# Optimization experiments

Measured on AMD Instinct MI355X. Metric: run time of the kernel, lower is better.

## Reference

```python
import jax, jax.numpy as jnp
import numpy as np

# Grid spacing (CartesianGrid3D.dx / .dy)
DX = 1000.0
DY = 1000.0
WENO_EPS = 1e-6  # classic Jiang-Shu smoothness regularizer

NZ, NY, NX = 32, 1024, 1024


def _weno5_recon(qm2, qm1, q0, qp1, qp2):
    """Classic WENO5 (Jiang-Shu) reconstruction of q at the i+1/2 face,
    left-biased (stencil centered on cell i)."""
    c1312 = 13.0 / 12.0
    b0 = c1312 * (qm2 - 2.0 * qm1 + q0) ** 2 + 0.25 * (qm2 - 4.0 * qm1 + 3.0 * q0) ** 2
    b1 = c1312 * (qm1 - 2.0 * q0 + qp1) ** 2 + 0.25 * (qm1 - qp1) ** 2
    b2 = c1312 * (q0 - 2.0 * qp1 + qp2) ** 2 + 0.25 * (3.0 * q0 - 4.0 * qp1 + qp2) ** 2
    a0 = 0.1 / (WENO_EPS + b0) ** 2
    a1 = 0.6 / (WENO_EPS + b1) ** 2
    a2 = 0.3 / (WENO_EPS + b2) ** 2
    p0 = (2.0 * qm2 - 7.0 * qm1 + 11.0 * q0) / 6.0
    p1 = (-qm1 + 5.0 * q0 + 2.0 * qp1) / 6.0
    p2 = (2.0 * q0 + 5.0 * qp1 - qp2) / 6.0
    return (a0 * p0 + a1 * p1 + a2 * p2) / (a0 + a1 + a2)


def _weno5_flux(q, vel, axis):
    """Upwinded WENO5 flux vel * q_face at face i+1/2 along `axis`.
    Edge-padded so the flux array has the same shape as q (faithful to
    recon.weno5_x / weno5_y producing full-shape flux arrays whose interior
    is consumed by the divergence)."""
    q = jnp.moveaxis(q, axis, -1)
    vel = jnp.moveaxis(vel, axis, -1)
    n = q.shape[-1]
    pad = [(0, 0)] * (q.ndim - 1) + [(2, 3)]
    qp = jnp.pad(q, pad, mode='edge')
    sl = lambda o: qp[..., o:o + n]
    qm2, qm1, q0, qp1, qp2, qp3 = sl(0), sl(1), sl(2), sl(3), sl(4), sl(5)
    q_left = _weno5_recon(qm2, qm1, q0, qp1, qp2)          # upwind for vel >= 0
    q_right = _weno5_recon(qp3, qp2, qp1, q0, qm1)         # mirrored, vel < 0
    f = vel * jnp.where(vel >= 0.0, q_left, q_right)
    return jnp.moveaxis(f, -1, axis)


def setup_inputs() -> dict:
    key = jax.random.key(0)
    kh, ku, kv = jax.random.split(key, 3)
    h = jax.random.normal(kh, (NZ, NY, NX), dtype=jnp.float32)
    u = jax.random.normal(ku, (NZ, NY, NX), dtype=jnp.float32)
    v = jax.random.normal(kv, (NZ, NY, NX), dtype=jnp.float32)
    return {"h": h, "u": u, "v": v}


def reference(h, u, v):
    # fe: flux through east face (x), fn: flux through north face (y)
    fe = _weno5_flux(h, u, axis=2)
    fn = _weno5_flux(h, v, axis=1)
    div = ((fe[1:-1, 2:-2, 2:-2] - fe[1:-1, 2:-2, 1:-3]) / DX
           + (fn[1:-1, 2:-2, 2:-2] - fn[1:-1, 1:-3, 2:-2]) / DY)
    out = jnp.zeros_like(h)
    out = out.at[1:-1, 2:-2, 2:-2].set(-div)
    return out
```

## Files before the change

### kernel.cpp

```cpp
#include <hip/hip_runtime.h>

#define NZ 32
#define NY 1024
#define NX 1024

__device__ __forceinline__ float rcpf(float x) { return __builtin_amdgcn_rcpf(x); }

__device__ __forceinline__ float weno5(float qm2, float qm1, float q0, float qp1, float qp2) {
    const float c1312 = 13.0f / 12.0f;
    float t0 = qm2 - 2.0f * qm1 + q0;
    float u0 = qm2 - 4.0f * qm1 + 3.0f * q0;
    float b0 = c1312 * t0 * t0 + 0.25f * u0 * u0;
    float t1 = qm1 - 2.0f * q0 + qp1;
    float u1 = qm1 - qp1;
    float b1 = c1312 * t1 * t1 + 0.25f * u1 * u1;
    float t2 = q0 - 2.0f * qp1 + qp2;
    float u2 = 3.0f * q0 - 4.0f * qp1 + qp2;
    float b2 = c1312 * t2 * t2 + 0.25f * u2 * u2;
    float e0 = 1e-6f + b0;
    float e1 = 1e-6f + b1;
    float e2 = 1e-6f + b2;
    float a0 = 0.1f * rcpf(e0 * e0);
    float a1 = 0.6f * rcpf(e1 * e1);
    float a2 = 0.3f * rcpf(e2 * e2);
    const float c16 = 1.0f / 6.0f;
    float p0 = (2.0f * qm2 - 7.0f * qm1 + 11.0f * q0) * c16;
    float p1 = (-qm1 + 5.0f * q0 + 2.0f * qp1) * c16;
    float p2 = (2.0f * q0 + 5.0f * qp1 - qp2) * c16;
    return (a0 * p0 + a1 * p1 + a2 * p2) * rcpf(a0 + a1 + a2);
}

__device__ __forceinline__ float upwind_flux(float vel, float qm2, float qm1, float q0,
                                             float qp1, float qp2, float qp3) {
    bool up = vel >= 0.0f;
    float s0 = up ? qm2 : qp3;
    float s1 = up ? qm1 : qp2;
    float s2 = up ? q0  : qp1;
    float s3 = up ? qp1 : q0;
    float s4 = up ? qp2 : qm1;
    return vel * weno5(s0, s1, s2, s3, s4);
}

__global__ __launch_bounds__(256) void adv_kernel(const float* __restrict__ h,
                                                  const float* __restrict__ u,
                                                  const float* __restrict__ v,
                                                  float* __restrict__ out) {
    int x = blockIdx.x * blockDim.x + threadIdx.x;
    int y = blockIdx.y;
    int z = blockIdx.z;
    size_t base = ((size_t)z * NY + y) * NX;
    size_t idx = base + x;

    bool interior = (z >= 1) && (z <= NZ - 2) && (y >= 2) && (y <= NY - 3) &&
                    (x >= 2) && (x <= NX - 3);
    if (!interior) {
        out[idx] = 0.0f;
        return;
    }

    const float* row = h + base;
    float hx[7];
#pragma unroll
    for (int k = 0; k < 7; ++k) {
        int xx = x - 3 + k;
        xx = xx < 0 ? 0 : (xx > NX - 1 ? NX - 1 : xx);
        hx[k] = row[xx];
    }
    float fe_hi = upwind_flux(u[idx],     hx[1], hx[2], hx[3], hx[4], hx[5], hx[6]);
    float fe_lo = upwind_flux(u[idx - 1], hx[0], hx[1], hx[2], hx[3], hx[4], hx[5]);

    float hy[7];
#pragma unroll
    for (int k = 0; k < 7; ++k) {
        int yy = y - 3 + k;
        yy = yy < 0 ? 0 : (yy > NY - 1 ? NY - 1 : yy);
        hy[k] = h[((size_t)z * NY + yy) * NX + x];
    }
    float fn_hi = upwind_flux(v[idx],      hy[1], hy[2], hy[3], hy[4], hy[5], hy[6]);
    float fn_lo = upwind_flux(v[idx - NX], hy[0], hy[1], hy[2], hy[3], hy[4], hy[5]);

    const float inv_dx = 1.0f / 1000.0f;
    const float inv_dy = 1.0f / 1000.0f;
    out[idx] = -((fe_hi - fe_lo) * inv_dx + (fn_hi - fn_lo) * inv_dy);
}

extern "C" void kernel_launch(void* const* d_in, const int* in_sizes, int n_in,
                              void* d_out, int out_size, void* d_ws, size_t ws_size,
                              hipStream_t stream) {
    const float* h = (const float*)d_in[0];
    const float* u = (const float*)d_in[1];
    const float* v = (const float*)d_in[2];
    float* out = (float*)d_out;

    dim3 block(256, 1, 1);
    dim3 grid(NX / 256, NY, NZ);
    adv_kernel<<<grid, block, 0, stream>>>(h, u, v, out);
}
```

Measured before the change: 444.2 us.

## Tile h in shared memory, reuse face fluxes across rows and cells

Each block now processes 8 rows and stages an h tile with a 3-cell halo in LDS. Each x-face and y-face flux is computed once and shared between neighbouring cells, instead of being computed twice per cell (hi and lo). The WENO weights are also rewritten to use products of the other smoothness terms, which avoids three reciprocals. This removes redundant WENO evaluations and repeated global loads, at the cost of LDS use, two barriers and more registers. Without the regularised reciprocal, products of squared betas can overflow or underflow.

```diff
diff --git a/kernel.cpp b/kernel.cpp
--- a/kernel.cpp
+++ b/kernel.cpp
@@ -3,6 +3,10 @@
 #define NZ 32
 #define NY 1024
 #define NX 1024
+#define KY 8
+#define BX 256
+#define HS 264
+#define FS 258
 
 __device__ __forceinline__ float rcpf(float x) { return __builtin_amdgcn_rcpf(x); }
 
@@ -17,12 +21,11 @@
     float t2 = q0 - 2.0f * qp1 + qp2;
     float u2 = 3.0f * q0 - 4.0f * qp1 + qp2;
     float b2 = c1312 * t2 * t2 + 0.25f * u2 * u2;
-    float e0 = 1e-6f + b0;
-    float e1 = 1e-6f + b1;
-    float e2 = 1e-6f + b2;
-    float a0 = 0.1f * rcpf(e0 * e0);
-    float a1 = 0.6f * rcpf(e1 * e1);
-    float a2 = 0.3f * rcpf(e2 * e2);
+    float e0 = 1e-6f + b0, e1 = 1e-6f + b1, e2 = 1e-6f + b2;
+    float s12 = e1 * e2, s02 = e0 * e2, s01 = e0 * e1;
+    float a0 = 0.1f * (s12 * s12);
+    float a1 = 0.6f * (s02 * s02);
+    float a2 = 0.3f * (s01 * s01);
     const float c16 = 1.0f / 6.0f;
     float p0 = (2.0f * qm2 - 7.0f * qm1 + 11.0f * q0) * c16;
     float p1 = (-qm1 + 5.0f * q0 + 2.0f * qp1) * c16;
@@ -41,47 +44,80 @@
     return vel * weno5(s0, s1, s2, s3, s4);
 }
 
+__device__ __forceinline__ int clampi(int a, int lo, int hi) {
+    return a < lo ? lo : (a > hi ? hi : a);
+}
+
 __global__ __launch_bounds__(256) void adv_kernel(const float* __restrict__ h,
                                                   const float* __restrict__ u,
                                                   const float* __restrict__ v,
                                                   float* __restrict__ out) {
-    int x = blockIdx.x * blockDim.x + threadIdx.x;
-    int y = blockIdx.y;
-    int z = blockIdx.z;
-    size_t base = ((size_t)z * NY + y) * NX;
-    size_t idx = base + x;
+    __shared__ float hs[(KY + 6) * HS];
+    __shared__ float fs[KY * FS];
 
-    bool interior = (z >= 1) && (z <= NZ - 2) && (y >= 2) && (y <= NY - 3) &&
-                    (x >= 2) && (x <= NX - 3);
-    if (!interior) {
-        out[idx] = 0.0f;
+    const int tid = threadIdx.x;
+    const int x0 = blockIdx.x * BX;
+    const int y0 = blockIdx.y * KY;
+    const int z  = blockIdx.z;
+    const int x = x0 + tid;
+    const size_t zbase = (size_t)z * NY * NX;
+
+    if (z == 0 || z == NZ - 1) {
+#pragma unroll
+        for (int r = 0; r < KY; ++r)
+            out[zbase + (size_t)(y0 + r) * NX + x] = 0.0f;
         return;
     }
 
-    const float* row = h + base;
-    float hx[7];
 #pragma unroll
-    for (int k = 0; k < 7; ++k) {
-        int xx = x - 3 + k;
-        xx = xx < 0 ? 0 : (xx > NX - 1 ? NX - 1 : xx);
-        hx[k] = row[xx];
+    for (int r = 0; r < KY + 6; ++r) {
+        int yy = clampi(y0 - 3 + r, 0, NY - 1);
+        const float* hrow = h + zbase + (size_t)yy * NX;
+        for (int c = tid; c < HS; c += BX) {
+            int xx = clampi(x0 - 3 + c, 0, NX - 1);
+            hs[r * HS + c] = hrow[xx];
+        }
     }
-    float fe_hi = upwind_flux(u[idx],     hx[1], hx[2], hx[3], hx[4], hx[5], hx[6]);
-    float fe_lo = upwind_flux(u[idx - 1], hx[0], hx[1], hx[2], hx[3], hx[4], hx[5]);
+    __syncthreads();
 
-    float hy[7];
+    float hc[KY + 6];
 #pragma unroll
-    for (int k = 0; k < 7; ++k) {
-        int yy = y - 3 + k;
-        yy = yy < 0 ? 0 : (yy > NY - 1 ? NY - 1 : yy);
-        hy[k] = h[((size_t)z * NY + yy) * NX + x];
+    for (int k = 0; k < KY + 6; ++k) hc[k] = hs[k * HS + tid + 3];
+
+    float fnf[KY + 1];
+#pragma unroll
+    for (int j = 0; j <= KY; ++j) {
+        int yy = clampi(y0 - 1 + j, 0, NY - 1);
+        float vv = v[zbase + (size_t)yy * NX + x];
+        fnf[j] = upwind_flux(vv, hc[j], hc[j + 1], hc[j + 2], hc[j + 3], hc[j + 4], hc[j + 5]);
     }
-    float fn_hi = upwind_flux(v[idx],      hy[1], hy[2], hy[3], hy[4], hy[5], hy[6]);
-    float fn_lo = upwind_flux(v[idx - NX], hy[0], hy[1], hy[2], hy[3], hy[4], hy[5]);
 
-    const float inv_dx = 1.0f / 1000.0f;
-    const float inv_dy = 1.0f / 1000.0f;
-    out[idx] = -((fe_hi - fe_lo) * inv_dx + (fn_hi - fn_lo) * inv_dy);
+#pragma unroll
+    for (int r = 0; r < KY; ++r) {
+        float uu = u[zbase + (size_t)(y0 + r) * NX + x];
+        const float* hr = &hs[(3 + r) * HS + tid];
+        fs[r * FS + tid + 1] = upwind_flux(uu, hr[1], hr[2], hr[3], hr[4], hr[5], hr[6]);
+    }
+    if ((tid & 31) == 0) {
+        int r = tid >> 5;
+        int xw = x0 > 0 ? x0 - 1 : 0;
+        float uu = u[zbase + (size_t)(y0 + r) * NX + xw];
+        const float* hr = &hs[(3 + r) * HS];
+        fs[r * FS] = upwind_flux(uu, hr[0], hr[1], hr[2], hr[3], hr[4], hr[5]);
+    }
+    __syncthreads();
+
+    const float inv_d = 1.0f / 1000.0f;
+    const bool xin = (x >= 2) && (x <= NX - 3);
+#pragma unroll
+    for (int r = 0; r < KY; ++r) {
+        int y = y0 + r;
+        float fe_hi = fs[r * FS + tid + 1];
+        float fe_lo = fs[r * FS + tid];
+        float val = -((fe_hi - fe_lo) + (fnf[r + 1] - fnf[r])) * inv_d;
+        bool in = xin && (y >= 2) && (y <= NY - 3);
+        out[zbase + (size_t)y * NX + x] = in ? val : 0.0f;
+    }
 }
 
 extern "C" void kernel_launch(void* const* d_in, const int* in_sizes, int n_in,
@@ -92,7 +128,7 @@
     const float* v = (const float*)d_in[2];
     float* out = (float*)d_out;
 
-    dim3 block(256, 1, 1);
-    dim3 grid(NX / 256, NY, NZ);
+    dim3 block(BX, 1, 1);
+    dim3 grid(NX / BX, NY / KY, NZ);
     adv_kernel<<<grid, block, 0, stream>>>(h, u, v, out);
 }
```

Result: slower. 461.8 us (+4.0%).
